# Kernel tuning notes

Measured on AMD Instinct MI355X. Metric: run time of the kernel, lower is better.

Reference implementation:

```python
import jax, jax.numpy as jnp
import numpy as np

N_NODES = 100000
N_EDGES = 3200000
D = 256


def setup_inputs() -> dict:
    key = jax.random.key(0)
    k1, k2, k3, k4, k5, k6 = jax.random.split(key, 6)
    embeddings = jax.random.normal(k1, (N_NODES, D), dtype=jnp.float32)
    edge_vals = jax.random.uniform(k2, (N_EDGES,), dtype=jnp.float32)
    # glorot-ish scale for the dense transforms
    scale = 1.0 / np.sqrt(D)
    W1 = jax.random.normal(k3, (D, D), dtype=jnp.float32) * scale
    W2 = jax.random.normal(k4, (D, D), dtype=jnp.float32) * scale
    edge_rows = jax.random.randint(k5, (N_EDGES,), 0, N_NODES, dtype=jnp.int32)
    edge_cols = jax.random.randint(k6, (N_EDGES,), 0, N_NODES, dtype=jnp.int32)
    return {
        "embeddings": embeddings,
        "edge_vals": edge_vals,
        "W1": W1,
        "W2": W2,
        "edge_rows": edge_rows,
        "edge_cols": edge_cols,
    }


def reference(embeddings, edge_vals, W1, W2, edge_rows, edge_cols):
    # SpMM: neighbor_interaction = A @ embeddings, A given as COO (rows, cols, vals)
    gathered = edge_vals[:, None] * embeddings[edge_cols]          # [E, D]
    neighbor = jax.ops.segment_sum(gathered, edge_rows,
                                   num_segments=embeddings.shape[0])  # [N, D]
    # include_self_messages = True branch:
    # self_interaction + neighbor_messages  ==  (emb + neighbor) @ W1
    out = (embeddings + neighbor) @ W1 + (neighbor * embeddings) @ W2
    return out
```

## Files before the change

kernel.cpp:

```cpp
#include <hip/hip_runtime.h>
#include <cstdint>
#include <cstddef>

#define N_NODES 100000
#define N_EDGES 3200000
#define DD 256
#define KK 512
#define MPAD 100096
#define NSCAN 98

typedef __attribute__((ext_vector_type(8))) __bf16 bf16x8;
typedef __attribute__((ext_vector_type(4))) __bf16 bf16x4;
typedef __attribute__((ext_vector_type(4))) float f32x4;

__device__ __forceinline__ void gload_lds16(const void* gsrc, void* lds) {
  __builtin_amdgcn_global_load_lds((const __attribute__((address_space(1))) void*)gsrc,
                                   (__attribute__((address_space(3))) void*)lds,
                                   16, 0, 0);
}


__global__ void conve_kernel(const float* __restrict__ emb, __bf16* __restrict__ embB) {
  int i = blockIdx.x * blockDim.x + threadIdx.x;
  float4 v = ((const float4*)emb)[i];
  bf16x4 o;
  o[0] = (__bf16)v.x; o[1] = (__bf16)v.y; o[2] = (__bf16)v.z; o[3] = (__bf16)v.w;
  ((bf16x4*)embB)[i] = o;
}

__global__ void convw_kernel(const float* __restrict__ W1, const float* __restrict__ W2,
                             __bf16* __restrict__ Wt) {
  int idx = blockIdx.x * blockDim.x + threadIdx.x;
  int n = idx >> 9;
  int k = idx & 511;
  float v = (k < 256) ? W1[k * 256 + n] : W2[(k - 256) * 256 + n];
  Wt[idx] = (__bf16)v;
}


__global__ void zero_ints_kernel(int* __restrict__ p, int n) {
  int i = blockIdx.x * blockDim.x + threadIdx.x;
  if (i < n) p[i] = 0;
}

__global__ void hist_kernel(const int* __restrict__ rows, int* __restrict__ counts, int e) {
  int i = blockIdx.x * blockDim.x + threadIdx.x;
  int stride = gridDim.x * blockDim.x;
  for (; i < e; i += stride) atomicAdd(&counts[rows[i]], 1);
}

__global__ void scan_block_kernel(const int* __restrict__ counts, int* __restrict__ offsets,
                                  int* __restrict__ blockSums, int n) {
  __shared__ int s[1024];
  int t = threadIdx.x;
  int i = blockIdx.x * 1024 + t;
  int v = (i < n) ? counts[i] : 0;
  s[t] = v;
  __syncthreads();
  for (int off = 1; off < 1024; off <<= 1) {
    int x = (t >= off) ? s[t - off] : 0;
    __syncthreads();
    s[t] += x;
    __syncthreads();
  }
  if (i < n) offsets[i + 1] = s[t];
  if (t == 1023) blockSums[blockIdx.x] = s[1023];
}

__global__ void scan_sums_kernel(const int* __restrict__ blockSums, int* __restrict__ blockBase,
                                 int nb, int* __restrict__ offsets) {
  __shared__ int s[128];
  int t = threadIdx.x;
  int v = (t < nb) ? blockSums[t] : 0;
  s[t] = v;
  __syncthreads();
  for (int off = 1; off < 128; off <<= 1) {
    int x = (t >= off) ? s[t - off] : 0;
    __syncthreads();
    s[t] += x;
    __syncthreads();
  }
  if (t < nb) blockBase[t] = s[t] - v;
  if (t == 0) offsets[0] = 0;
}

__global__ void scan_add_kernel(const int* __restrict__ counts, int* __restrict__ offsets,
                                const int* __restrict__ blockBase, int* __restrict__ cursor, int n) {
  int i = blockIdx.x * 1024 + threadIdx.x;
  if (i < n) {
    int incl = offsets[i + 1] + blockBase[blockIdx.x];
    offsets[i + 1] = incl;
    cursor[i] = incl - counts[i];
  }
}

__global__ void bin_kernel(const int* __restrict__ rows, const int* __restrict__ cols,
                           const float* __restrict__ vals, int* __restrict__ cursor,
                           int* __restrict__ scol, float* __restrict__ sval, int e) {
  int i = blockIdx.x * blockDim.x + threadIdx.x;
  int stride = gridDim.x * blockDim.x;
  for (; i < e; i += stride) {
    int r = rows[i];
    int pos = atomicAdd(&cursor[r], 1);
    scol[pos] = cols[i];
    sval[pos] = vals[i];
  }
}


__global__ void spmm_fuse_kernel(const __bf16* __restrict__ embB, const int* __restrict__ offsets,
                                 const int* __restrict__ scol, const float* __restrict__ sval,
                                 __bf16* __restrict__ X) {
  int gw = (blockIdx.x << 2) + (threadIdx.x >> 6);
  int lane = threadIdx.x & 63;
  bf16x4* xp1 = (bf16x4*)(X + (size_t)gw * KK + 4 * lane);
  bf16x4* xp2 = (bf16x4*)(X + (size_t)gw * KK + DD + 4 * lane);
  if (gw >= N_NODES) {
    bf16x4 z;
    z[0] = (__bf16)0.f; z[1] = (__bf16)0.f; z[2] = (__bf16)0.f; z[3] = (__bf16)0.f;
    *xp1 = z; *xp2 = z;
    return;
  }
  const bf16x4* ev = (const bf16x4*)embB;
  float ax = 0.f, ay = 0.f, az = 0.f, aw = 0.f;
  int e = offsets[gw];
  const int eend = offsets[gw + 1];
  for (; e + 3 < eend; e += 4) {
    int c0 = scol[e], c1 = scol[e + 1], c2 = scol[e + 2], c3 = scol[e + 3];
    float v0 = sval[e], v1 = sval[e + 1], v2 = sval[e + 2], v3 = sval[e + 3];
    bf16x4 x0 = ev[(size_t)c0 * 64 + lane];
    bf16x4 x1 = ev[(size_t)c1 * 64 + lane];
    bf16x4 x2 = ev[(size_t)c2 * 64 + lane];
    bf16x4 x3 = ev[(size_t)c3 * 64 + lane];
    ax = fmaf(v0, (float)x0[0], ax); ay = fmaf(v0, (float)x0[1], ay);
    az = fmaf(v0, (float)x0[2], az); aw = fmaf(v0, (float)x0[3], aw);
    ax = fmaf(v1, (float)x1[0], ax); ay = fmaf(v1, (float)x1[1], ay);
    az = fmaf(v1, (float)x1[2], az); aw = fmaf(v1, (float)x1[3], aw);
    ax = fmaf(v2, (float)x2[0], ax); ay = fmaf(v2, (float)x2[1], ay);
    az = fmaf(v2, (float)x2[2], az); aw = fmaf(v2, (float)x2[3], aw);
    ax = fmaf(v3, (float)x3[0], ax); ay = fmaf(v3, (float)x3[1], ay);
    az = fmaf(v3, (float)x3[2], az); aw = fmaf(v3, (float)x3[3], aw);
  }
  for (; e < eend; ++e) {
    int c = scol[e];
    float v = sval[e];
    bf16x4 x = ev[(size_t)c * 64 + lane];
    ax = fmaf(v, (float)x[0], ax); ay = fmaf(v, (float)x[1], ay);
    az = fmaf(v, (float)x[2], az); aw = fmaf(v, (float)x[3], aw);
  }
  bf16x4 er = ev[(size_t)gw * 64 + lane];
  float ex = (float)er[0], ey = (float)er[1], ez = (float)er[2], ew = (float)er[3];
  bf16x4 o1, o2;
  o1[0] = (__bf16)(ex + ax); o1[1] = (__bf16)(ey + ay);
  o1[2] = (__bf16)(ez + az); o1[3] = (__bf16)(ew + aw);
  o2[0] = (__bf16)(ex * ax); o2[1] = (__bf16)(ey * ay);
  o2[2] = (__bf16)(ez * az); o2[3] = (__bf16)(ew * aw);
  *xp1 = o1;
  *xp2 = o2;
}


__global__ __launch_bounds__(256) void gemm_kernel(const __bf16* __restrict__ X,
                                                   const __bf16* __restrict__ Wt,
                                                   float* __restrict__ out) {
  __shared__ __align__(16) __bf16 As[128 * 64];
  __shared__ __align__(16) __bf16 Bs[128 * 64];
  const int t = threadIdx.x;
  const int w = t >> 6, lane = t & 63;
  const int m0 = blockIdx.x * 128;
  const int n0 = blockIdx.y * 128;
  const int wm = (w >> 1) * 64, wn = (w & 1) * 64;
  const int lrow = lane >> 3, lcol = lane & 7;

  f32x4 acc[4][4];
#pragma unroll
  for (int i = 0; i < 4; ++i)
#pragma unroll
    for (int j = 0; j < 4; ++j) {
      f32x4 z = {0.f, 0.f, 0.f, 0.f};
      acc[i][j] = z;
    }

  for (int kt = 0; kt < KK; kt += 64) {
#pragma unroll
    for (int q = 0; q < 4; ++q) {
      const int cbase = w * 256 + q * 64;
      const int arow = m0 + w * 32 + q * 8 + lrow;
      gload_lds16(X + (size_t)arow * KK + kt + lcol * 8, (char*)As + cbase * 16);
      const int brow = n0 + w * 32 + q * 8 + lrow;
      gload_lds16(Wt + (size_t)brow * KK + kt + lcol * 8, (char*)Bs + cbase * 16);
    }
    __syncthreads();
#pragma unroll
    for (int kk = 0; kk < 64; kk += 32) {
      const int ko = kk + (lane >> 4) * 8;
      bf16x8 af[4], bg[4];
#pragma unroll
      for (int i = 0; i < 4; ++i)
        af[i] = *(const bf16x8*)(As + (wm + i * 16 + (lane & 15)) * 64 + ko);
#pragma unroll
      for (int j = 0; j < 4; ++j)
        bg[j] = *(const bf16x8*)(Bs + (wn + j * 16 + (lane & 15)) * 64 + ko);
#pragma unroll
      for (int i = 0; i < 4; ++i)
#pragma unroll
        for (int j = 0; j < 4; ++j)
          acc[i][j] = __builtin_amdgcn_mfma_f32_16x16x32_bf16(af[i], bg[j], acc[i][j], 0, 0, 0);
    }
    __syncthreads();
  }

  const int orow0 = m0 + wm + ((lane >> 4) << 2);
  const int ocol0 = n0 + wn + (lane & 15);
#pragma unroll
  for (int i = 0; i < 4; ++i)
#pragma unroll
    for (int j = 0; j < 4; ++j)
#pragma unroll
      for (int r = 0; r < 4; ++r) {
        const int row = orow0 + i * 16 + r;
        if (row < N_NODES) out[(size_t)row * DD + ocol0 + j * 16] = acc[i][j][r];
      }
}


extern "C" void kernel_launch(void* const* d_in, const int* in_sizes, int n_in,
                              void* d_out, int out_size, void* d_ws, size_t ws_size,
                              hipStream_t stream) {
  const float* emb  = (const float*)d_in[0];
  const float* ev   = (const float*)d_in[1];
  const float* W1   = (const float*)d_in[2];
  const float* W2   = (const float*)d_in[3];
  const int* erows  = (const int*)d_in[4];
  const int* ecols  = (const int*)d_in[5];
  float* out = (float*)d_out;
  char* ws = (char*)d_ws;

  const size_t OFF_X   = 0;
  const size_t OFF_EMB = OFF_X   + (size_t)MPAD * KK * 2;
  const size_t OFF_WT  = OFF_EMB + (size_t)N_NODES * DD * 2;
  const size_t OFF_CNT = OFF_WT  + (size_t)KK * DD * 2;
  const size_t OFF_OFS = OFF_CNT + 401408;
  const size_t OFF_CUR = OFF_OFS + 401408;
  const size_t OFF_BS  = OFF_CUR + 401408;
  const size_t OFF_BB  = OFF_BS  + 4096;
  const size_t OFF_SC  = OFF_BB  + 4096;
  const size_t OFF_SV  = OFF_SC  + (size_t)N_EDGES * 4;

  __bf16* X     = (__bf16*)(ws + OFF_X);
  __bf16* embB  = (__bf16*)(ws + OFF_EMB);
  __bf16* Wt    = (__bf16*)(ws + OFF_WT);
  int* counts   = (int*)(ws + OFF_CNT);
  int* offsets  = (int*)(ws + OFF_OFS);
  int* cursor   = (int*)(ws + OFF_CUR);
  int* bsums    = (int*)(ws + OFF_BS);
  int* bbase    = (int*)(ws + OFF_BB);
  int* scol     = (int*)(ws + OFF_SC);
  float* sval   = (float*)(ws + OFF_SV);

  conve_kernel<<<(N_NODES * 64) / 256, 256, 0, stream>>>(emb, embB);
  convw_kernel<<<(KK * DD) / 256, 256, 0, stream>>>(W1, W2, Wt);

  zero_ints_kernel<<<(N_NODES + 255) / 256, 256, 0, stream>>>(counts, N_NODES);
  hist_kernel<<<2048, 256, 0, stream>>>(erows, counts, N_EDGES);
  scan_block_kernel<<<NSCAN, 1024, 0, stream>>>(counts, offsets, bsums, N_NODES);
  scan_sums_kernel<<<1, 128, 0, stream>>>(bsums, bbase, NSCAN, offsets);
  scan_add_kernel<<<NSCAN, 1024, 0, stream>>>(counts, offsets, bbase, cursor, N_NODES);
  bin_kernel<<<2048, 256, 0, stream>>>(erows, ecols, ev, cursor, scol, sval, N_EDGES);

  spmm_fuse_kernel<<<MPAD / 4, 256, 0, stream>>>(embB, offsets, scol, sval, X);

  gemm_kernel<<<dim3(MPAD / 128, 2), 256, 0, stream>>>(X, Wt, out);

  (void)in_sizes; (void)n_in; (void)out_size; (void)ws_size;
}
```

Measured before the change: 829.0 us.

## Pack sorted edges as uint2 and partition binning by row group

Col and val are now scattered together into one interleaved uint2 array, so each bin write is one 8-byte store and SpMM reads one record per edge instead of two separate arrays. The bin kernel now splits edges into 256 slots and rows into 8 groups. Each block scans one slot and only scatters edges whose row falls in its group, so atomics and writes for a block hit a narrower cursor and output range. In exchange, the rows array is read 8 times, once per group.

```diff
diff --git a/kernel.cpp b/kernel.cpp
--- a/kernel.cpp
+++ b/kernel.cpp
@@ -8,6 +8,10 @@
 #define KK 512
 #define MPAD 100096
 #define NSCAN 98
+#define NGRP 8
+#define GRP_ROWS 12500
+#define NSLOT 256
+#define SLOT_E 12500
 
 typedef __attribute__((ext_vector_type(8))) __bf16 bf16x8;
 typedef __attribute__((ext_vector_type(4))) __bf16 bf16x4;
@@ -96,21 +100,24 @@
 
 __global__ void bin_kernel(const int* __restrict__ rows, const int* __restrict__ cols,
                            const float* __restrict__ vals, int* __restrict__ cursor,
-                           int* __restrict__ scol, float* __restrict__ sval, int e) {
-  int i = blockIdx.x * blockDim.x + threadIdx.x;
-  int stride = gridDim.x * blockDim.x;
-  for (; i < e; i += stride) {
+                           uint2* __restrict__ sedge) {
+  const int g = blockIdx.x & (NGRP - 1);
+  const int s = blockIdx.x >> 3;
+  const int rlo = g * GRP_ROWS;
+  const int rhi = rlo + GRP_ROWS;
+  const int base = s * SLOT_E;
+  for (int i = base + threadIdx.x; i < base + SLOT_E; i += 256) {
     int r = rows[i];
-    int pos = atomicAdd(&cursor[r], 1);
-    scol[pos] = cols[i];
-    sval[pos] = vals[i];
+    if (r >= rlo && r < rhi) {
+      int pos = atomicAdd(&cursor[r], 1);
+      sedge[pos] = make_uint2((unsigned)cols[i], __float_as_uint(vals[i]));
+    }
   }
 }
 
 
 __global__ void spmm_fuse_kernel(const __bf16* __restrict__ embB, const int* __restrict__ offsets,
-                                 const int* __restrict__ scol, const float* __restrict__ sval,
-                                 __bf16* __restrict__ X) {
+                                 const uint2* __restrict__ sedge, __bf16* __restrict__ X) {
   int gw = (blockIdx.x << 2) + (threadIdx.x >> 6);
   int lane = threadIdx.x & 63;
   bf16x4* xp1 = (bf16x4*)(X + (size_t)gw * KK + 4 * lane);
@@ -126,12 +133,13 @@
   int e = offsets[gw];
   const int eend = offsets[gw + 1];
   for (; e + 3 < eend; e += 4) {
-    int c0 = scol[e], c1 = scol[e + 1], c2 = scol[e + 2], c3 = scol[e + 3];
-    float v0 = sval[e], v1 = sval[e + 1], v2 = sval[e + 2], v3 = sval[e + 3];
-    bf16x4 x0 = ev[(size_t)c0 * 64 + lane];
-    bf16x4 x1 = ev[(size_t)c1 * 64 + lane];
-    bf16x4 x2 = ev[(size_t)c2 * 64 + lane];
-    bf16x4 x3 = ev[(size_t)c3 * 64 + lane];
+    uint2 e0 = sedge[e], e1 = sedge[e + 1], e2 = sedge[e + 2], e3 = sedge[e + 3];
+    float v0 = __uint_as_float(e0.y), v1 = __uint_as_float(e1.y);
+    float v2 = __uint_as_float(e2.y), v3 = __uint_as_float(e3.y);
+    bf16x4 x0 = ev[(size_t)e0.x * 64 + lane];
+    bf16x4 x1 = ev[(size_t)e1.x * 64 + lane];
+    bf16x4 x2 = ev[(size_t)e2.x * 64 + lane];
+    bf16x4 x3 = ev[(size_t)e3.x * 64 + lane];
     ax = fmaf(v0, (float)x0[0], ax); ay = fmaf(v0, (float)x0[1], ay);
     az = fmaf(v0, (float)x0[2], az); aw = fmaf(v0, (float)x0[3], aw);
     ax = fmaf(v1, (float)x1[0], ax); ay = fmaf(v1, (float)x1[1], ay);
@@ -142,9 +150,9 @@
     az = fmaf(v3, (float)x3[2], az); aw = fmaf(v3, (float)x3[3], aw);
   }
   for (; e < eend; ++e) {
-    int c = scol[e];
-    float v = sval[e];
-    bf16x4 x = ev[(size_t)c * 64 + lane];
+    uint2 ee = sedge[e];
+    float v = __uint_as_float(ee.y);
+    bf16x4 x = ev[(size_t)ee.x * 64 + lane];
     ax = fmaf(v, (float)x[0], ax); ay = fmaf(v, (float)x[1], ay);
     az = fmaf(v, (float)x[2], az); aw = fmaf(v, (float)x[3], aw);
   }
@@ -244,8 +252,7 @@
   const size_t OFF_CUR = OFF_OFS + 401408;
   const size_t OFF_BS  = OFF_CUR + 401408;
   const size_t OFF_BB  = OFF_BS  + 4096;
-  const size_t OFF_SC  = OFF_BB  + 4096;
-  const size_t OFF_SV  = OFF_SC  + (size_t)N_EDGES * 4;
+  const size_t OFF_SE  = OFF_BB  + 4096;
 
   __bf16* X     = (__bf16*)(ws + OFF_X);
   __bf16* embB  = (__bf16*)(ws + OFF_EMB);
@@ -255,8 +262,7 @@
   int* cursor   = (int*)(ws + OFF_CUR);
   int* bsums    = (int*)(ws + OFF_BS);
   int* bbase    = (int*)(ws + OFF_BB);
-  int* scol     = (int*)(ws + OFF_SC);
-  float* sval   = (float*)(ws + OFF_SV);
+  uint2* sedge  = (uint2*)(ws + OFF_SE);
 
   conve_kernel<<<(N_NODES * 64) / 256, 256, 0, stream>>>(emb, embB);
   convw_kernel<<<(KK * DD) / 256, 256, 0, stream>>>(W1, W2, Wt);
@@ -266,9 +272,9 @@
   scan_block_kernel<<<NSCAN, 1024, 0, stream>>>(counts, offsets, bsums, N_NODES);
   scan_sums_kernel<<<1, 128, 0, stream>>>(bsums, bbase, NSCAN, offsets);
   scan_add_kernel<<<NSCAN, 1024, 0, stream>>>(counts, offsets, bbase, cursor, N_NODES);
-  bin_kernel<<<2048, 256, 0, stream>>>(erows, ecols, ev, cursor, scol, sval, N_EDGES);
-
-  spmm_fuse_kernel<<<MPAD / 4, 256, 0, stream>>>(embB, offsets, scol, sval, X);
+  bin_kernel<<<NGRP * NSLOT, 256, 0, stream>>>(erows, ecols, ev, cursor, sedge);
+
+  spmm_fuse_kernel<<<MPAD / 4, 256, 0, stream>>>(embB, offsets, sedge, X);
 
   gemm_kernel<<<dim3(MPAD / 128, 2), 256, 0, stream>>>(X, Wt, out);
 
```

New measurement: 770.5 us. 7.1% less time.
